# Performance work log

Measured on AMD Instinct MI355X. Metric: run time of the kernel, lower is better.

The kernel has to match this reference:

```python
import jax, jax.numpy as jnp
import numpy as np

B, C, T, E = 8, 512, 2048, 512
LN_EPS = 1e-5


def setup_inputs() -> dict:
    key = jax.random.key(0)
    ks = jax.random.split(key, 12)
    std = 0.02
    return {
        "x": jax.random.normal(ks[0], (B, C, T), dtype=jnp.float32),
        "Wq": jax.random.normal(ks[1], (C, E), dtype=jnp.float32) * std,
        "bq": jnp.zeros((E,), dtype=jnp.float32),
        "Wk": jax.random.normal(ks[2], (C, E), dtype=jnp.float32) * std,
        "bk": jnp.zeros((E,), dtype=jnp.float32),
        "Wv": jax.random.normal(ks[3], (C, E), dtype=jnp.float32) * std,
        "bv": jnp.zeros((E,), dtype=jnp.float32),
        "Wo": jax.random.normal(ks[4], (E, C), dtype=jnp.float32) * std,
        "bo": jnp.zeros((C,), dtype=jnp.float32),
        "gamma": jnp.ones((C,), dtype=jnp.float32),
        "beta": jnp.zeros((C,), dtype=jnp.float32),
    }


def reference(x, Wq, bq, Wk, bk, Wv, bv, Wo, bo, gamma, beta):
    # x: [B, C, T] channels-first -> residual [B, T, C]
    residual = jnp.transpose(x, (0, 2, 1))
    q = residual @ Wq + bq            # [B, T, E]
    k = residual @ Wk + bk            # [B, T, E]
    v = residual @ Wv + bv            # [B, T, E]
    # Unscaled dot-product attention (no 1/sqrt(E) in the original)
    energy = jnp.einsum("bte,bse->bts", q, k)         # [B, T, T]
    attn = jax.nn.softmax(energy, axis=-1)             # [B, T, T]
    attended = jnp.einsum("bts,bse->bte", attn, v)    # [B, T, E]
    attended = attended @ Wo + bo                      # [B, T, C]
    h = attended + residual                            # residual add
    # LayerNorm over last dim (C)
    mu = jnp.mean(h, axis=-1, keepdims=True)
    var = jnp.mean(jnp.square(h - mu), axis=-1, keepdims=True)
    out = (h - mu) * jax.lax.rsqrt(var + LN_EPS) * gamma + beta
    return attn, out
```

## Files before the change

### kernel.cpp

```cpp
#include <hip/hip_runtime.h>

#define B_ 8
#define C_ 512
#define T_ 2048
#define E_ 512
#define LN_EPS 1e-5f

typedef __attribute__((ext_vector_type(8))) short bf16x8;
typedef __attribute__((ext_vector_type(4))) float f32x4;

__device__ __forceinline__ unsigned short f2bf(float f) {
  union { float f; unsigned u; } v; v.f = f;
  unsigned u = v.u;
  u += 0x7fff + ((u >> 16) & 1);
  return (unsigned short)(u >> 16);
}
__device__ __forceinline__ float bf2f(unsigned short h) {
  union { unsigned u; float f; } v; v.u = ((unsigned)h) << 16;
  return v.f;
}

__device__ __forceinline__ void gl2lds16(const unsigned short* g, unsigned short* l) {
  __builtin_amdgcn_global_load_lds(
      (const __attribute__((address_space(1))) unsigned int*)g,
      (__attribute__((address_space(3))) unsigned int*)l, 16, 0, 0);
}

__global__ __launch_bounds__(256) void transpose_x(const float* __restrict__ x,
    unsigned short* __restrict__ rb) {
  __shared__ float tile[32][33];
  int b = blockIdx.z;
  int t0 = blockIdx.x * 32, c0 = blockIdx.y * 32;
  int tx = threadIdx.x, ty = threadIdx.y;
  const float* xb = x + (long)b * C_ * T_;
#pragma unroll
  for (int i = 0; i < 4; i++)
    tile[ty + i * 8][tx] = xb[(long)(c0 + ty + i * 8) * T_ + t0 + tx];
  __syncthreads();
  long ob = (long)b * T_ * C_;
#pragma unroll
  for (int i = 0; i < 4; i++)
    rb[ob + (long)(t0 + ty + i * 8) * C_ + c0 + tx] = f2bf(tile[tx][ty + i * 8]);
}

__global__ __launch_bounds__(256) void transpose_w(const float* __restrict__ W,
    unsigned short* __restrict__ Wt) {
  __shared__ float tile[32][33];
  int e0 = blockIdx.x * 32, c0 = blockIdx.y * 32;
  int tx = threadIdx.x, ty = threadIdx.y;
#pragma unroll
  for (int i = 0; i < 4; i++)
    tile[ty + i * 8][tx] = W[(long)(c0 + ty + i * 8) * E_ + e0 + tx];
  __syncthreads();
#pragma unroll
  for (int i = 0; i < 4; i++)
    Wt[(long)(e0 + ty + i * 8) * C_ + c0 + tx] = f2bf(tile[tx][ty + i * 8]);
}

__global__ void concat_bias(const float* __restrict__ bq, const float* __restrict__ bk,
                            float* __restrict__ bqk) {
  int i = blockIdx.x * 256 + threadIdx.x;
  bqk[i] = (i < 512) ? bq[i] : bk[i - 512];
}

template<int EPI>
__global__ __launch_bounds__(256) void gemm_bt(
    const unsigned short* __restrict__ Ap, const unsigned short* __restrict__ Btp,
    unsigned short* __restrict__ Cp, const float* __restrict__ bias,
    const unsigned short* __restrict__ resid,
    int K, int lda, int ldb, int ldc, long sA, long sB, long sC) {
  __shared__ unsigned short As[128 * 32];
  __shared__ unsigned short Bs[128 * 32];
  const int b = blockIdx.z;
  const int tid = threadIdx.x;
  const int lane = tid & 63, wave = tid >> 6;
  const int wr = (wave >> 1) * 64, wc = (wave & 1) * 64;
  const int quad = lane >> 4, l16 = lane & 15;
  const long m0 = (long)blockIdx.y * 128, n0 = (long)blockIdx.x * 128;
  const unsigned short* A  = Ap  + (long)b * sA;
  const unsigned short* Bt = Btp + (long)b * sB;

  const int srow = lane >> 2;
  const int soff = (lane & 3) * 8;
  const int ra = wave * 32;
  const unsigned short* ga = A  + (m0 + ra + srow) * (long)lda + soff;
  const unsigned short* gb = Bt + (n0 + ra + srow) * (long)ldb + soff;
  unsigned short* la0 = &As[ra * 32];
  unsigned short* la1 = &As[(ra + 16) * 32];
  unsigned short* lb0 = &Bs[ra * 32];
  unsigned short* lb1 = &Bs[(ra + 16) * 32];

  f32x4 acc[4][4] = {};

  for (int k0 = 0; k0 < K; k0 += 32) {
    __syncthreads();
    gl2lds16(ga + k0, la0);
    gl2lds16(ga + 16 * (long)lda + k0, la1);
    gl2lds16(gb + k0, lb0);
    gl2lds16(gb + 16 * (long)ldb + k0, lb1);
    __syncthreads();
    bf16x8 af[4], bfr[4];
#pragma unroll
    for (int i = 0; i < 4; i++)
      af[i] = *(const bf16x8*)&As[(wr + i * 16 + l16) * 32 + quad * 8];
#pragma unroll
    for (int j = 0; j < 4; j++)
      bfr[j] = *(const bf16x8*)&Bs[(wc + j * 16 + l16) * 32 + quad * 8];
#pragma unroll
    for (int i = 0; i < 4; i++)
#pragma unroll
      for (int j = 0; j < 4; j++)
        acc[i][j] = __builtin_amdgcn_mfma_f32_16x16x32_bf16(af[i], bfr[j], acc[i][j], 0, 0, 0);
  }

  const long cb = (long)b * sC;
#pragma unroll
  for (int i = 0; i < 4; i++) {
#pragma unroll
    for (int rr = 0; rr < 4; rr++) {
      const long m = m0 + wr + i * 16 + quad * 4 + rr;
#pragma unroll
      for (int j = 0; j < 4; j++) {
        const long n = n0 + wc + j * 16 + l16;
        float v = acc[i][j][rr];
        if (EPI == 0) v += bias[n];
        else if (EPI == 1) v += bias[m];
        else if (EPI == 2) v += bias[n] + bf2f(resid[m * (long)ldc + n]);
        Cp[cb + m * (long)ldc + n] = f2bf(v);
      }
    }
  }
}

__global__ __launch_bounds__(256) void softmax_rows(unsigned short* __restrict__ eb,
                                                    float* __restrict__ attn) {
  long row = blockIdx.x;
  unsigned short* p = eb + row * (long)T_;
  float* o = attn + row * (long)T_;
  int tid = threadIdx.x;
  bf16x8 raw = *(const bf16x8*)(p + tid * 8);
  float vals[8];
  float mx = -1e30f;
#pragma unroll
  for (int i = 0; i < 8; i++) {
    vals[i] = bf2f((unsigned short)raw[i]);
    mx = fmaxf(mx, vals[i]);
  }
#pragma unroll
  for (int o2 = 32; o2 > 0; o2 >>= 1) mx = fmaxf(mx, __shfl_xor(mx, o2, 64));
  __shared__ float red[4];
  if ((tid & 63) == 0) red[tid >> 6] = mx;
  __syncthreads();
  mx = fmaxf(fmaxf(red[0], red[1]), fmaxf(red[2], red[3]));
  float sum = 0.f;
#pragma unroll
  for (int i = 0; i < 8; i++) { vals[i] = __expf(vals[i] - mx); sum += vals[i]; }
#pragma unroll
  for (int o2 = 32; o2 > 0; o2 >>= 1) sum += __shfl_xor(sum, o2, 64);
  __shared__ float red2[4];
  if ((tid & 63) == 0) red2[tid >> 6] = sum;
  __syncthreads();
  sum = red2[0] + red2[1] + red2[2] + red2[3];
  float inv = 1.f / sum;
  unsigned short ob[8];
  float r0[4], r1[4];
#pragma unroll
  for (int i = 0; i < 8; i++) {
    float r = vals[i] * inv;
    if (i < 4) r0[i] = r; else r1[i - 4] = r;
    ob[i] = f2bf(r);
  }
  *(float4*)(o + tid * 8)     = *(float4*)r0;
  *(float4*)(o + tid * 8 + 4) = *(float4*)r1;
  *(bf16x8*)(p + tid * 8) = *(bf16x8*)ob;
}

__global__ __launch_bounds__(256) void layernorm_rows(const unsigned short* __restrict__ hb,
    const float* __restrict__ gamma, const float* __restrict__ beta,
    float* __restrict__ out) {
  long row = blockIdx.x;
  const unsigned short* p = hb + row * C_;
  int tid = threadIdx.x;
  unsigned pr = *(const unsigned*)(p + 2 * tid);
  float v0 = bf2f((unsigned short)(pr & 0xffff));
  float v1 = bf2f((unsigned short)(pr >> 16));
  float s = v0 + v1, sq = v0 * v0 + v1 * v1;
#pragma unroll
  for (int o = 32; o > 0; o >>= 1) { s += __shfl_xor(s, o, 64); sq += __shfl_xor(sq, o, 64); }
  __shared__ float rs[4], rq[4];
  if ((tid & 63) == 0) { rs[tid >> 6] = s; rq[tid >> 6] = sq; }
  __syncthreads();
  s = rs[0] + rs[1] + rs[2] + rs[3];
  sq = rq[0] + rq[1] + rq[2] + rq[3];
  float mu = s * (1.f / 512.f);
  float var = sq * (1.f / 512.f) - mu * mu;
  float rstd = rsqrtf(var + LN_EPS);
  out[row * C_ + 2 * tid]     = (v0 - mu) * rstd * gamma[2 * tid] + beta[2 * tid];
  out[row * C_ + 2 * tid + 1] = (v1 - mu) * rstd * gamma[2 * tid + 1] + beta[2 * tid + 1];
}

extern "C" void kernel_launch(void* const* d_in, const int* in_sizes, int n_in,
                              void* d_out, int out_size, void* d_ws, size_t ws_size,
                              hipStream_t stream) {
  const float* x  = (const float*)d_in[0];
  const float* Wq = (const float*)d_in[1];
  const float* bq = (const float*)d_in[2];
  const float* Wk = (const float*)d_in[3];
  const float* bk = (const float*)d_in[4];
  const float* Wv = (const float*)d_in[5];
  const float* bv = (const float*)d_in[6];
  const float* Wo = (const float*)d_in[7];
  const float* bo = (const float*)d_in[8];
  const float* gamma = (const float*)d_in[9];
  const float* beta  = (const float*)d_in[10];
  float* out = (float*)d_out;

  char* ws = (char*)d_ws;
  unsigned short* res_b = (unsigned short*)ws;
  unsigned short* qk    = (unsigned short*)(ws + (16ul << 20));
  unsigned short* att   = (unsigned short*)(ws + (16ul << 20));
  unsigned short* hb    = (unsigned short*)(ws + (32ul << 20));
  unsigned short* vt    = (unsigned short*)(ws + (48ul << 20));
  unsigned short* eb    = (unsigned short*)(ws + (64ul << 20));
  unsigned short* WqkT  = (unsigned short*)(ws + (128ul << 20));
  unsigned short* WvT   = (unsigned short*)(ws + (130ul << 20));
  unsigned short* WoT   = (unsigned short*)(ws + (130ul << 20) + 524288);
  float*          bqk   = (float*)(ws + (131ul << 20));

  float* attn_f = out;
  float* outln  = out + (long)B_ * T_ * T_;

  dim3 tb(32, 8);
  transpose_x<<<dim3(T_ / 32, C_ / 32, B_), tb, 0, stream>>>(x, res_b);
  transpose_w<<<dim3(16, 16), tb, 0, stream>>>(Wq, WqkT);
  transpose_w<<<dim3(16, 16), tb, 0, stream>>>(Wk, WqkT + 512 * 512);
  transpose_w<<<dim3(16, 16), tb, 0, stream>>>(Wv, WvT);
  transpose_w<<<dim3(16, 16), tb, 0, stream>>>(Wo, WoT);
  concat_bias<<<dim3(4), 256, 0, stream>>>(bq, bk, bqk);

  gemm_bt<0><<<dim3(8, 128, 1), 256, 0, stream>>>(
      res_b, WqkT, qk, bqk, nullptr, 512, 512, 512, 1024, 0L, 0L, 0L);
  gemm_bt<1><<<dim3(16, 4, B_), 256, 0, stream>>>(
      WvT, res_b, vt, bv, nullptr, 512, 512, 512, 2048,
      0L, (long)T_ * C_, 512L * 2048);
  gemm_bt<4><<<dim3(16, 16, B_), 256, 0, stream>>>(
      qk, qk + 512, eb, nullptr, nullptr, 512, 1024, 1024, 2048,
      (long)T_ * 1024, (long)T_ * 1024, (long)T_ * T_);
  softmax_rows<<<dim3(B_ * T_), 256, 0, stream>>>(eb, attn_f);
  gemm_bt<4><<<dim3(4, 16, B_), 256, 0, stream>>>(
      eb, vt, att, nullptr, nullptr, 2048, 2048, 2048, 512,
      (long)T_ * T_, 512L * 2048, (long)T_ * 512);
  gemm_bt<2><<<dim3(4, 128, 1), 256, 0, stream>>>(
      att, WoT, hb, bo, res_b, 512, 512, 512, 512, 0L, 0L, 0L);
  layernorm_rows<<<dim3(B_ * T_), 256, 0, stream>>>(hb, gamma, beta, outln);
}
```

Measured before the change: 454.6 us.

## Use K=64 tiles with XOR-swizzled LDS and templated row-tile size in GEMM

The bf16 MFMA GEMM now stages K=64 slices instead of 32 per iteration, halving barrier pairs per K. The LDS layout is XOR-swizzled on 16-byte chunks so fragment reads avoid bank conflicts. A BM template parameter lets the smaller GEMMs (V projection, attention-times-V, output projection) use 64-row tiles, doubling their grid size for better CU occupancy. LDS use per block grows, and smaller tiles lower per-block data reuse.

```diff
diff --git a/kernel.cpp b/kernel.cpp
--- a/kernel.cpp
+++ b/kernel.cpp
@@ -63,59 +63,60 @@
   bqk[i] = (i < 512) ? bq[i] : bk[i - 512];
 }
 
-template<int EPI>
+template<int EPI, int BM>
 __global__ __launch_bounds__(256) void gemm_bt(
     const unsigned short* __restrict__ Ap, const unsigned short* __restrict__ Btp,
     unsigned short* __restrict__ Cp, const float* __restrict__ bias,
     const unsigned short* __restrict__ resid,
     int K, int lda, int ldb, int ldc, long sA, long sB, long sC) {
-  __shared__ unsigned short As[128 * 32];
-  __shared__ unsigned short Bs[128 * 32];
+  __shared__ unsigned short As[BM * 64];
+  __shared__ unsigned short Bs[128 * 64];
+  constexpr int WI = BM / 32;
   const int b = blockIdx.z;
   const int tid = threadIdx.x;
   const int lane = tid & 63, wave = tid >> 6;
-  const int wr = (wave >> 1) * 64, wc = (wave & 1) * 64;
+  const int wr = (wave >> 1) * (BM / 2);
+  const int wc = (wave & 1) * 64;
   const int quad = lane >> 4, l16 = lane & 15;
-  const long m0 = (long)blockIdx.y * 128, n0 = (long)blockIdx.x * 128;
-  const unsigned short* A  = Ap  + (long)b * sA;
-  const unsigned short* Bt = Btp + (long)b * sB;
-
-  const int srow = lane >> 2;
-  const int soff = (lane & 3) * 8;
-  const int ra = wave * 32;
-  const unsigned short* ga = A  + (m0 + ra + srow) * (long)lda + soff;
-  const unsigned short* gb = Bt + (n0 + ra + srow) * (long)ldb + soff;
-  unsigned short* la0 = &As[ra * 32];
-  unsigned short* la1 = &As[(ra + 16) * 32];
-  unsigned short* lb0 = &Bs[ra * 32];
-  unsigned short* lb1 = &Bs[(ra + 16) * 32];
-
-  f32x4 acc[4][4] = {};
-
-  for (int k0 = 0; k0 < K; k0 += 32) {
+  const long m0 = (long)blockIdx.y * BM, n0 = (long)blockIdx.x * 128;
+
+  const int srow = lane >> 3;
+  const int gcol = ((lane & 7) ^ srow) * 8;
+  const unsigned short* ga = Ap + (long)b * sA + (m0 + srow) * (long)lda + gcol;
+  const unsigned short* gb = Btp + (long)b * sB + (n0 + srow) * (long)ldb + gcol;
+
+  f32x4 acc[WI][4] = {};
+
+  for (int k0 = 0; k0 < K; k0 += 64) {
     __syncthreads();
-    gl2lds16(ga + k0, la0);
-    gl2lds16(ga + 16 * (long)lda + k0, la1);
-    gl2lds16(gb + k0, lb0);
-    gl2lds16(gb + 16 * (long)ldb + k0, lb1);
+#pragma unroll
+    for (int s = 0; s < WI; s++)
+      gl2lds16(ga + (s * 32 + wave * 8) * (long)lda + k0, &As[(s * 32 + wave * 8) * 64]);
+#pragma unroll
+    for (int s = 0; s < 4; s++)
+      gl2lds16(gb + (s * 32 + wave * 8) * (long)ldb + k0, &Bs[(s * 32 + wave * 8) * 64]);
     __syncthreads();
-    bf16x8 af[4], bfr[4];
-#pragma unroll
-    for (int i = 0; i < 4; i++)
-      af[i] = *(const bf16x8*)&As[(wr + i * 16 + l16) * 32 + quad * 8];
-#pragma unroll
-    for (int j = 0; j < 4; j++)
-      bfr[j] = *(const bf16x8*)&Bs[(wc + j * 16 + l16) * 32 + quad * 8];
-#pragma unroll
-    for (int i = 0; i < 4; i++)
+#pragma unroll
+    for (int ks = 0; ks < 2; ks++) {
+      const int cs = ((ks * 4 + quad) ^ (l16 & 7)) * 8;
+      bf16x8 af[WI], bfr[4];
+#pragma unroll
+      for (int i = 0; i < WI; i++)
+        af[i] = *(const bf16x8*)&As[(wr + i * 16 + l16) * 64 + cs];
 #pragma unroll
       for (int j = 0; j < 4; j++)
-        acc[i][j] = __builtin_amdgcn_mfma_f32_16x16x32_bf16(af[i], bfr[j], acc[i][j], 0, 0, 0);
+        bfr[j] = *(const bf16x8*)&Bs[(wc + j * 16 + l16) * 64 + cs];
+#pragma unroll
+      for (int i = 0; i < WI; i++)
+#pragma unroll
+        for (int j = 0; j < 4; j++)
+          acc[i][j] = __builtin_amdgcn_mfma_f32_16x16x32_bf16(af[i], bfr[j], acc[i][j], 0, 0, 0);
+    }
   }
 
   const long cb = (long)b * sC;
 #pragma unroll
-  for (int i = 0; i < 4; i++) {
+  for (int i = 0; i < WI; i++) {
 #pragma unroll
     for (int rr = 0; rr < 4; rr++) {
       const long m = m0 + wr + i * 16 + quad * 4 + rr;
@@ -238,19 +239,19 @@
   transpose_w<<<dim3(16, 16), tb, 0, stream>>>(Wo, WoT);
   concat_bias<<<dim3(4), 256, 0, stream>>>(bq, bk, bqk);
 
-  gemm_bt<0><<<dim3(8, 128, 1), 256, 0, stream>>>(
+  gemm_bt<0, 128><<<dim3(8, 128, 1), 256, 0, stream>>>(
       res_b, WqkT, qk, bqk, nullptr, 512, 512, 512, 1024, 0L, 0L, 0L);
-  gemm_bt<1><<<dim3(16, 4, B_), 256, 0, stream>>>(
+  gemm_bt<1, 64><<<dim3(16, 8, B_), 256, 0, stream>>>(
       WvT, res_b, vt, bv, nullptr, 512, 512, 512, 2048,
       0L, (long)T_ * C_, 512L * 2048);
-  gemm_bt<4><<<dim3(16, 16, B_), 256, 0, stream>>>(
+  gemm_bt<4, 128><<<dim3(16, 16, B_), 256, 0, stream>>>(
       qk, qk + 512, eb, nullptr, nullptr, 512, 1024, 1024, 2048,
       (long)T_ * 1024, (long)T_ * 1024, (long)T_ * T_);
   softmax_rows<<<dim3(B_ * T_), 256, 0, stream>>>(eb, attn_f);
-  gemm_bt<4><<<dim3(4, 16, B_), 256, 0, stream>>>(
+  gemm_bt<4, 64><<<dim3(4, 32, B_), 256, 0, stream>>>(
       eb, vt, att, nullptr, nullptr, 2048, 2048, 2048, 512,
       (long)T_ * T_, 512L * 2048, (long)T_ * 512);
-  gemm_bt<2><<<dim3(4, 128, 1), 256, 0, stream>>>(
+  gemm_bt<2, 64><<<dim3(4, 256, 1), 256, 0, stream>>>(
       att, WoT, hb, bo, res_b, 512, 512, 512, 512, 0L, 0L, 0L);
   layernorm_rows<<<dim3(B_ * T_), 256, 0, stream>>>(hb, gamma, beta, outln);
 }
```

After: 423.7 us. -6.8%, faster.
